# Kernel tuning notes

Hardware: AMD Instinct MI355X
Metric: run time of the kernel (lower is better)

## Reference

```python
import jax, jax.numpy as jnp
import numpy as np

B, S, I, R, O = 32, 4096, 64, 1024, 8
SPECTRAL_RADIUS = 0.95


def setup_inputs() -> dict:
    key = jax.random.key(0)
    k1, k2, k3, k4 = jax.random.split(key, 4)
    x = jax.random.normal(k1, (B, S, I), dtype=jnp.float32)
    W_in = jax.random.uniform(k2, (R, I), dtype=jnp.float32) - 0.5
    W_res = jax.random.uniform(k3, (R, R), dtype=jnp.float32) - 0.5
    # rescale W_res so its spectral radius equals SPECTRAL_RADIUS (as in __init__)
    radius = SPECTRAL_RADIUS / float(np.max(np.abs(np.linalg.eigvals(np.asarray(W_res)))))
    W_res = W_res * jnp.float32(radius)
    # original inits W_out to zeros; use small random values so output is non-trivial
    W_out = jax.random.normal(k4, (O, R + I), dtype=jnp.float32) * 0.02
    return {"x": x, "W_in": W_in, "W_res": W_res, "W_out": W_out}


def reference(x, W_in, W_res, W_out):
    # Precompute input drive for all timesteps: [B, S, R]
    pre = jnp.einsum('bsi,ri->bsr', x, W_in)

    def step(r, p_t):
        # r: [B, R], p_t: [B, R]
        r = jnp.tanh(p_t + r @ W_res.T)
        return r, r

    r0 = jnp.zeros((x.shape[0], W_res.shape[0]), dtype=x.dtype)
    _, rs = jax.lax.scan(step, r0, jnp.swapaxes(pre, 0, 1))  # rs: [S, B, R]
    rs = jnp.swapaxes(rs, 0, 1)                               # [B, S, R]
    feats = jnp.concatenate([x, rs], axis=-1)                 # [B, S, I+R]
    out = jnp.einsum('bsf,of->bso', feats, W_out)             # [B, S, O]
    return jnp.squeeze(out)
```

## Files before the change

### kernel.cpp

```cpp
#include <hip/hip_runtime.h>
#include <hip/hip_fp16.h>
#include <math.h>


#define NS 4096
#define NI 64
#define NR 1024
#define NO 8
#define NB 32
#define NGRP 8
#define GPP 32
#define CPG 4
#define WROWS 32
#define NT 512
#define XPAD 68

typedef __fp16 h2 __attribute__((ext_vector_type(2)));
union UH2 { unsigned u; h2 h; };

#define ATSU(p,v) __hip_atomic_store((p), (v), __ATOMIC_RELAXED, __HIP_MEMORY_SCOPE_AGENT)
#define ATLU(p)   __hip_atomic_load((p), __ATOMIC_RELAXED, __HIP_MEMORY_SCOPE_AGENT)
#define ATAU(p,v) __hip_atomic_fetch_add((p), (v), __ATOMIC_RELAXED, __HIP_MEMORY_SCOPE_AGENT)

static __device__ __forceinline__ h2 u2h(unsigned u) { UH2 t; t.u = u; return t.h; }

__global__ void init_cnt_kernel(unsigned int* cnt) {
  cnt[threadIdx.x] = 0u;
  cnt[threadIdx.x + 1024] = 0u;
}

__global__ __launch_bounds__(NT)
__attribute__((amdgpu_waves_per_eu(2, 2)))
void esn_scan(const float* __restrict__ x, const float* __restrict__ Win,
              const float* __restrict__ Wres, const float* __restrict__ Wout,
              float* __restrict__ out, unsigned int* __restrict__ cnt,
              unsigned int* __restrict__ rbuf_h)
{
  extern __shared__ float dynpad[];
  const int wg  = blockIdx.x;
  const int g   = wg & 7;
  const int m   = wg >> 3;
  const int tid = threadIdx.x;
  const int w   = tid >> 6;
  const int l   = tid & 63;

  __shared__ unsigned r_h[CPG][NR / 2];
  __shared__ float x_lds[3][CPG][XPAD];
  __shared__ float win_s[WROWS][XPAD];
  __shared__ unsigned woutr_h[NO][NR / 2];
  __shared__ float woutx_s[NO][NI];

  if (x[0] == 1234.5678f) { dynpad[tid] = 1.f; out[tid] = dynpad[tid ^ 1]; }

  h2 wh[32];
  {
    const int grow0 = 32 * m + 4 * w;
    #pragma unroll
    for (int r = 0; r < 4; ++r)
      #pragma unroll
      for (int s = 0; s < 4; ++s) {
        float4 t4 = *(const float4*)&Wres[(size_t)(grow0 + r) * NR + 4 * l + 256 * s];
        wh[(r * 4 + s) * 2 + 0] = __builtin_amdgcn_cvt_pkrtz(t4.x, t4.y);
        wh[(r * 4 + s) * 2 + 1] = __builtin_amdgcn_cvt_pkrtz(t4.z, t4.w);
      }
  }
  for (int idx = tid; idx < WROWS * NI; idx += NT) {
    int rr = idx >> 6, ii = idx & 63;
    win_s[rr][ii] = Win[(32 * m + rr) * NI + ii];
  }
  for (int idx = tid; idx < NO * (NR / 2); idx += NT) {
    int o = idx >> 9, p = idx & 511;
    UH2 t; t.h = __builtin_amdgcn_cvt_pkrtz(Wout[o * (NI + NR) + NI + 2 * p],
                                            Wout[o * (NI + NR) + NI + 2 * p + 1]);
    woutr_h[o][p] = t.u;
  }
  if (tid < NO * NI) {
    int o = tid >> 6, ii = tid & 63;
    woutx_s[o][ii] = Wout[o * (NI + NR) + ii];
  }
  if (tid < 256) {
    const int c = tid >> 6, ii = tid & 63;
    x_lds[0][c][ii] = x[(size_t)(4 * g + c) * NS * NI + ii];
  }
  __syncthreads();

  unsigned int* bcp = cnt + (g * 4 + (m & 3)) * 64;
  unsigned int* pol = cnt + g * 4 * 64;

  for (int t = 0; t < NS; ++t) {
    const int par = t & 1, pprev = par ^ 1;

    if (t > 0) {
      const unsigned* rq = rbuf_h + (size_t)pprev * NB * (NR / 2)
                                  + (size_t)(4 * g) * (NR / 2);
      unsigned uv[4];
      #pragma unroll
      for (int c = 0; c < 4; ++c) uv[c] = ATLU(rq + c * 512 + tid);
      #pragma unroll
      for (int c = 0; c < 4; ++c) r_h[c][tid] = uv[c];
    } else {
      #pragma unroll
      for (int c = 0; c < 4; ++c) r_h[c][tid] = 0u;
    }
    __syncthreads();

    float acc[4][4];
    #pragma unroll
    for (int r = 0; r < 4; ++r)
      #pragma unroll
      for (int c = 0; c < 4; ++c) acc[r][c] = 0.f;
    #pragma unroll
    for (int s = 0; s < 4; ++s) {
      uint2 q0 = *(const uint2*)&r_h[0][2 * l + 128 * s];
      uint2 q1 = *(const uint2*)&r_h[1][2 * l + 128 * s];
      uint2 q2 = *(const uint2*)&r_h[2][2 * l + 128 * s];
      uint2 q3 = *(const uint2*)&r_h[3][2 * l + 128 * s];
      #pragma unroll
      for (int r = 0; r < 4; ++r) {
        const h2 wa = wh[(r * 4 + s) * 2 + 0];
        const h2 wb = wh[(r * 4 + s) * 2 + 1];
        acc[r][0] = __builtin_amdgcn_fdot2(wa, u2h(q0.x), acc[r][0], false);
        acc[r][0] = __builtin_amdgcn_fdot2(wb, u2h(q0.y), acc[r][0], false);
        acc[r][1] = __builtin_amdgcn_fdot2(wa, u2h(q1.x), acc[r][1], false);
        acc[r][1] = __builtin_amdgcn_fdot2(wb, u2h(q1.y), acc[r][1], false);
        acc[r][2] = __builtin_amdgcn_fdot2(wa, u2h(q2.x), acc[r][2], false);
        acc[r][2] = __builtin_amdgcn_fdot2(wb, u2h(q2.y), acc[r][2], false);
        acc[r][3] = __builtin_amdgcn_fdot2(wa, u2h(q3.x), acc[r][3], false);
        acc[r][3] = __builtin_amdgcn_fdot2(wb, u2h(q3.y), acc[r][3], false);
      }
    }

    float v[16];
    #pragma unroll
    for (int k = 0; k < 16; ++k) v[k] = acc[k >> 2][k & 3];
    #pragma unroll
    for (int lev = 0; lev < 4; ++lev) {
      const int d = 1 << lev;
      const int n = 16 >> lev;
      #pragma unroll
      for (int i = 0; i < n / 2; ++i) {
        float a  = v[2 * i]     + __shfl_xor(v[2 * i],     d);
        float bb = v[2 * i + 1] + __shfl_xor(v[2 * i + 1], d);
        v[i] = (l & d) ? bb : a;
      }
    }
    float dsum = v[0];
    dsum += __shfl_xor(dsum, 16);
    dsum += __shfl_xor(dsum, 32);

    float pin;
    {
      const int p = l & 15;
      const int prow = 4 * w + (p >> 2);
      const int pc = p & 3;
      const int cb = (l >> 4) * 16;
      const float* wr = &win_s[prow][cb];
      const float* xr = &x_lds[t % 3][pc][cb];
      float4 a0 = *(const float4*)&wr[0];
      float4 a1 = *(const float4*)&wr[4];
      float4 a2 = *(const float4*)&wr[8];
      float4 a3 = *(const float4*)&wr[12];
      float4 b0 = *(const float4*)&xr[0];
      float4 b1 = *(const float4*)&xr[4];
      float4 b2 = *(const float4*)&xr[8];
      float4 b3 = *(const float4*)&xr[12];
      pin = a0.x * b0.x;
      pin = fmaf(a0.y, b0.y, pin); pin = fmaf(a0.z, b0.z, pin);
      pin = fmaf(a0.w, b0.w, pin);
      pin = fmaf(a1.x, b1.x, pin); pin = fmaf(a1.y, b1.y, pin);
      pin = fmaf(a1.z, b1.z, pin); pin = fmaf(a1.w, b1.w, pin);
      pin = fmaf(a2.x, b2.x, pin); pin = fmaf(a2.y, b2.y, pin);
      pin = fmaf(a2.z, b2.z, pin); pin = fmaf(a2.w, b2.w, pin);
      pin = fmaf(a3.x, b3.x, pin); pin = fmaf(a3.y, b3.y, pin);
      pin = fmaf(a3.z, b3.z, pin); pin = fmaf(a3.w, b3.w, pin);
      pin += __shfl_xor(pin, 16);
      pin += __shfl_xor(pin, 32);
    }

    {
      float rv = tanhf(dsum + pin);
      float rvo = __shfl_xor(rv, 4);
      if (l < 16 && ((l >> 2) & 1) == 0) {
        const int r = l >> 2, c = l & 3;
        UH2 hp; hp.h = __builtin_amdgcn_cvt_pkrtz(rv, rvo);
        const int pair = 16 * m + 2 * w + (r >> 1);
        ATSU(rbuf_h + (size_t)par * NB * (NR / 2)
                    + (size_t)(4 * g + c) * (NR / 2) + pair, hp.u);
      }
    }

    __syncthreads();
    if (tid == 0) ATAU(bcp, 1u);

    if (t + 1 < NS && tid < 256) {
      const int c = tid >> 6, ii = tid & 63;
      x_lds[(t + 1) % 3][c][ii] = x[((size_t)(4 * g + c) * NS + (t + 1)) * NI + ii];
    }
    if (t > 0 && m == ((t - 1) & 31)) {
      const int grp = tid >> 4;
      const int j   = tid & 15;
      const int c   = grp >> 3, o = grp & 7;
      float s = 0.f;
      #pragma unroll
      for (int k = 0; k < 16; ++k) {
        uint2 rr = *(const uint2*)&r_h[c][32 * k + 2 * j];
        uint2 ww = *(const uint2*)&woutr_h[o][32 * k + 2 * j];
        s = __builtin_amdgcn_fdot2(u2h(rr.x), u2h(ww.x), s, false);
        s = __builtin_amdgcn_fdot2(u2h(rr.y), u2h(ww.y), s, false);
      }
      #pragma unroll
      for (int e = 0; e < 4; ++e)
        s = fmaf(woutx_s[o][4 * j + e], x_lds[(t + 2) % 3][c][4 * j + e], s);
      s += __shfl_xor(s, 1); s += __shfl_xor(s, 2);
      s += __shfl_xor(s, 4); s += __shfl_xor(s, 8);
      if (j == 0) out[((size_t)(4 * g + c) * NS + (t - 1)) * NO + o] = s;
    }

    if (tid == 0) {
      const unsigned tg = 8u * (unsigned)(t + 1);
      for (;;) {
        unsigned u0 = ATLU(pol);
        unsigned u1 = ATLU(pol + 64);
        unsigned u2 = ATLU(pol + 128);
        unsigned u3 = ATLU(pol + 192);
        if (u0 >= tg && u1 >= tg && u2 >= tg && u3 >= tg) break;
      }
    }
    __syncthreads();
  }

  if (m == 31) {
    const int fpar = (NS - 1) & 1;
    const unsigned* rq = rbuf_h + (size_t)fpar * NB * (NR / 2)
                                + (size_t)(4 * g) * (NR / 2);
    unsigned uv[4];
    #pragma unroll
    for (int c = 0; c < 4; ++c) uv[c] = ATLU(rq + c * 512 + tid);
    #pragma unroll
    for (int c = 0; c < 4; ++c) r_h[c][tid] = uv[c];
    __syncthreads();
    const int grp = tid >> 4;
    const int j   = tid & 15;
    const int c   = grp >> 3, o = grp & 7;
    float s = 0.f;
    #pragma unroll
    for (int k = 0; k < 16; ++k) {
      uint2 rr = *(const uint2*)&r_h[c][32 * k + 2 * j];
      uint2 ww = *(const uint2*)&woutr_h[o][32 * k + 2 * j];
      s = __builtin_amdgcn_fdot2(u2h(rr.x), u2h(ww.x), s, false);
      s = __builtin_amdgcn_fdot2(u2h(rr.y), u2h(ww.y), s, false);
    }
    #pragma unroll
    for (int e = 0; e < 4; ++e)
      s = fmaf(woutx_s[o][4 * j + e], x_lds[(NS - 1) % 3][c][4 * j + e], s);
    s += __shfl_xor(s, 1); s += __shfl_xor(s, 2);
    s += __shfl_xor(s, 4); s += __shfl_xor(s, 8);
    if (j == 0) out[((size_t)(4 * g + c) * NS + (NS - 1)) * NO + o] = s;
  }
}

extern "C" void kernel_launch(void* const* d_in, const int* in_sizes, int n_in,
                              void* d_out, int out_size, void* d_ws, size_t ws_size,
                              hipStream_t stream) {
  const float* x    = (const float*)d_in[0];
  const float* Win  = (const float*)d_in[1];
  const float* Wres = (const float*)d_in[2];
  const float* Wout = (const float*)d_in[3];
  float* out = (float*)d_out;

  char* ws = (char*)d_ws;
  unsigned int* cnt = (unsigned int*)ws;
  unsigned int* rbuf_h = (unsigned int*)(ws + 8192);

  hipLaunchKernelGGL(init_cnt_kernel, dim3(1), dim3(1024), 0, stream, cnt);
  hipLaunchKernelGGL(esn_scan, dim3(256), dim3(NT), 64 * 1024, stream,
                     x, Win, Wres, Wout, out, cnt, rbuf_h);
}
```

Before: 10.12 ms.

## Interleave hidden-state buffer, widen barrier counters, overlap input GEMV, use fast tanh

The per-step hidden-state exchange buffer is interleaved across the 4 batch columns, so each thread reads 4 consecutive words instead of 4 strided ones. The inter-workgroup barrier goes from 4 counter slots per group to 8, each with fewer arrivals, and a whole wave polls them with a wave vote instead of one thread spinning. The x·W_in dot product is moved between the global load and the LDS store so it can hide the load latency. tanhf is replaced by an exp2/rcp approximation, which adds some rounding error.

```diff
diff --git a/kernel.cpp b/kernel.cpp
--- a/kernel.cpp
+++ b/kernel.cpp
@@ -14,6 +14,7 @@
 #define WROWS 32
 #define NT 512
 #define XPAD 68
+#define RPH (NB * NR / 2)
 
 typedef __fp16 h2 __attribute__((ext_vector_type(2)));
 union UH2 { unsigned u; h2 h; };
@@ -24,9 +25,15 @@
 
 static __device__ __forceinline__ h2 u2h(unsigned u) { UH2 t; t.u = u; return t.h; }
 
+static __device__ __forceinline__ float fast_tanh(float x) {
+  x = fminf(fmaxf(x, -20.f), 20.f);
+  float e = __builtin_amdgcn_exp2f(x * 2.8853900817779268f);
+  return (e - 1.0f) * __builtin_amdgcn_rcpf(e + 1.0f);
+}
+
 __global__ void init_cnt_kernel(unsigned int* cnt) {
-  cnt[threadIdx.x] = 0u;
-  cnt[threadIdx.x + 1024] = 0u;
+  const int t = threadIdx.x;
+  cnt[t] = 0u; cnt[t + 1024] = 0u; cnt[t + 2048] = 0u; cnt[t + 3072] = 0u;
 }
 
 __global__ __launch_bounds__(NT)
@@ -84,69 +91,19 @@
   }
   __syncthreads();
 
-  unsigned int* bcp = cnt + (g * 4 + (m & 3)) * 64;
-  unsigned int* pol = cnt + g * 4 * 64;
+  unsigned int* bcp = cnt + (g * 8 + (m & 7)) * 64;
 
   for (int t = 0; t < NS; ++t) {
     const int par = t & 1, pprev = par ^ 1;
 
+    unsigned uv0, uv1, uv2, uv3;
     if (t > 0) {
-      const unsigned* rq = rbuf_h + (size_t)pprev * NB * (NR / 2)
-                                  + (size_t)(4 * g) * (NR / 2);
-      unsigned uv[4];
-      #pragma unroll
-      for (int c = 0; c < 4; ++c) uv[c] = ATLU(rq + c * 512 + tid);
-      #pragma unroll
-      for (int c = 0; c < 4; ++c) r_h[c][tid] = uv[c];
+      const unsigned* rq = rbuf_h + (size_t)pprev * RPH + (size_t)g * 2048 + 4 * tid;
+      uv0 = ATLU(rq);     uv1 = ATLU(rq + 1);
+      uv2 = ATLU(rq + 2); uv3 = ATLU(rq + 3);
     } else {
-      #pragma unroll
-      for (int c = 0; c < 4; ++c) r_h[c][tid] = 0u;
-    }
-    __syncthreads();
-
-    float acc[4][4];
-    #pragma unroll
-    for (int r = 0; r < 4; ++r)
-      #pragma unroll
-      for (int c = 0; c < 4; ++c) acc[r][c] = 0.f;
-    #pragma unroll
-    for (int s = 0; s < 4; ++s) {
-      uint2 q0 = *(const uint2*)&r_h[0][2 * l + 128 * s];
-      uint2 q1 = *(const uint2*)&r_h[1][2 * l + 128 * s];
-      uint2 q2 = *(const uint2*)&r_h[2][2 * l + 128 * s];
-      uint2 q3 = *(const uint2*)&r_h[3][2 * l + 128 * s];
-      #pragma unroll
-      for (int r = 0; r < 4; ++r) {
-        const h2 wa = wh[(r * 4 + s) * 2 + 0];
-        const h2 wb = wh[(r * 4 + s) * 2 + 1];
-        acc[r][0] = __builtin_amdgcn_fdot2(wa, u2h(q0.x), acc[r][0], false);
-        acc[r][0] = __builtin_amdgcn_fdot2(wb, u2h(q0.y), acc[r][0], false);
-        acc[r][1] = __builtin_amdgcn_fdot2(wa, u2h(q1.x), acc[r][1], false);
-        acc[r][1] = __builtin_amdgcn_fdot2(wb, u2h(q1.y), acc[r][1], false);
-        acc[r][2] = __builtin_amdgcn_fdot2(wa, u2h(q2.x), acc[r][2], false);
-        acc[r][2] = __builtin_amdgcn_fdot2(wb, u2h(q2.y), acc[r][2], false);
-        acc[r][3] = __builtin_amdgcn_fdot2(wa, u2h(q3.x), acc[r][3], false);
-        acc[r][3] = __builtin_amdgcn_fdot2(wb, u2h(q3.y), acc[r][3], false);
-      }
-    }
-
-    float v[16];
-    #pragma unroll
-    for (int k = 0; k < 16; ++k) v[k] = acc[k >> 2][k & 3];
-    #pragma unroll
-    for (int lev = 0; lev < 4; ++lev) {
-      const int d = 1 << lev;
-      const int n = 16 >> lev;
-      #pragma unroll
-      for (int i = 0; i < n / 2; ++i) {
-        float a  = v[2 * i]     + __shfl_xor(v[2 * i],     d);
-        float bb = v[2 * i + 1] + __shfl_xor(v[2 * i + 1], d);
-        v[i] = (l & d) ? bb : a;
-      }
-    }
-    float dsum = v[0];
-    dsum += __shfl_xor(dsum, 16);
-    dsum += __shfl_xor(dsum, 32);
+      uv0 = uv1 = uv2 = uv3 = 0u;
+    }
 
     float pin;
     {
@@ -177,15 +134,62 @@
       pin += __shfl_xor(pin, 32);
     }
 
+    r_h[0][tid] = uv0; r_h[1][tid] = uv1;
+    r_h[2][tid] = uv2; r_h[3][tid] = uv3;
+    __syncthreads();
+
+    float acc[4][4];
+    #pragma unroll
+    for (int r = 0; r < 4; ++r)
+      #pragma unroll
+      for (int c = 0; c < 4; ++c) acc[r][c] = 0.f;
+    #pragma unroll
+    for (int s = 0; s < 4; ++s) {
+      uint2 q0 = *(const uint2*)&r_h[0][2 * l + 128 * s];
+      uint2 q1 = *(const uint2*)&r_h[1][2 * l + 128 * s];
+      uint2 q2 = *(const uint2*)&r_h[2][2 * l + 128 * s];
+      uint2 q3 = *(const uint2*)&r_h[3][2 * l + 128 * s];
+      #pragma unroll
+      for (int r = 0; r < 4; ++r) {
+        const h2 wa = wh[(r * 4 + s) * 2 + 0];
+        const h2 wb = wh[(r * 4 + s) * 2 + 1];
+        acc[r][0] = __builtin_amdgcn_fdot2(wa, u2h(q0.x), acc[r][0], false);
+        acc[r][0] = __builtin_amdgcn_fdot2(wb, u2h(q0.y), acc[r][0], false);
+        acc[r][1] = __builtin_amdgcn_fdot2(wa, u2h(q1.x), acc[r][1], false);
+        acc[r][1] = __builtin_amdgcn_fdot2(wb, u2h(q1.y), acc[r][1], false);
+        acc[r][2] = __builtin_amdgcn_fdot2(wa, u2h(q2.x), acc[r][2], false);
+        acc[r][2] = __builtin_amdgcn_fdot2(wb, u2h(q2.y), acc[r][2], false);
+        acc[r][3] = __builtin_amdgcn_fdot2(wa, u2h(q3.x), acc[r][3], false);
+        acc[r][3] = __builtin_amdgcn_fdot2(wb, u2h(q3.y), acc[r][3], false);
+      }
+    }
+
+    float v[16];
+    #pragma unroll
+    for (int k = 0; k < 16; ++k) v[k] = acc[k >> 2][k & 3];
+    #pragma unroll
+    for (int lev = 0; lev < 4; ++lev) {
+      const int d = 1 << lev;
+      const int n = 16 >> lev;
+      #pragma unroll
+      for (int i = 0; i < n / 2; ++i) {
+        float a  = v[2 * i]     + __shfl_xor(v[2 * i],     d);
+        float bb = v[2 * i + 1] + __shfl_xor(v[2 * i + 1], d);
+        v[i] = (l & d) ? bb : a;
+      }
+    }
+    float dsum = v[0];
+    dsum += __shfl_xor(dsum, 16);
+    dsum += __shfl_xor(dsum, 32);
+
     {
-      float rv = tanhf(dsum + pin);
+      float rv = fast_tanh(dsum + pin);
       float rvo = __shfl_xor(rv, 4);
       if (l < 16 && ((l >> 2) & 1) == 0) {
         const int r = l >> 2, c = l & 3;
         UH2 hp; hp.h = __builtin_amdgcn_cvt_pkrtz(rv, rvo);
         const int pair = 16 * m + 2 * w + (r >> 1);
-        ATSU(rbuf_h + (size_t)par * NB * (NR / 2)
-                    + (size_t)(4 * g + c) * (NR / 2) + pair, hp.u);
+        ATSU(rbuf_h + (size_t)par * RPH + (size_t)g * 2048 + 4 * pair + c, hp.u);
       }
     }
 
@@ -216,28 +220,21 @@
       if (j == 0) out[((size_t)(4 * g + c) * NS + (t - 1)) * NO + o] = s;
     }
 
-    if (tid == 0) {
-      const unsigned tg = 8u * (unsigned)(t + 1);
-      for (;;) {
-        unsigned u0 = ATLU(pol);
-        unsigned u1 = ATLU(pol + 64);
-        unsigned u2 = ATLU(pol + 128);
-        unsigned u3 = ATLU(pol + 192);
-        if (u0 >= tg && u1 >= tg && u2 >= tg && u3 >= tg) break;
-      }
+    if (w == 0) {
+      const unsigned tg = 4u * (unsigned)(t + 1);
+      const unsigned* pa = cnt + (g * 8 + (l & 7)) * 64;
+      while (!__all((int)(ATLU(pa) >= tg))) { }
     }
     __syncthreads();
   }
 
   if (m == 31) {
     const int fpar = (NS - 1) & 1;
-    const unsigned* rq = rbuf_h + (size_t)fpar * NB * (NR / 2)
-                                + (size_t)(4 * g) * (NR / 2);
-    unsigned uv[4];
-    #pragma unroll
-    for (int c = 0; c < 4; ++c) uv[c] = ATLU(rq + c * 512 + tid);
-    #pragma unroll
-    for (int c = 0; c < 4; ++c) r_h[c][tid] = uv[c];
+    const unsigned* rq = rbuf_h + (size_t)fpar * RPH + (size_t)g * 2048 + 4 * tid;
+    r_h[0][tid] = ATLU(rq);
+    r_h[1][tid] = ATLU(rq + 1);
+    r_h[2][tid] = ATLU(rq + 2);
+    r_h[3][tid] = ATLU(rq + 3);
     __syncthreads();
     const int grp = tid >> 4;
     const int j   = tid & 15;
@@ -270,7 +267,7 @@
 
   char* ws = (char*)d_ws;
   unsigned int* cnt = (unsigned int*)ws;
-  unsigned int* rbuf_h = (unsigned int*)(ws + 8192);
+  unsigned int* rbuf_h = (unsigned int*)(ws + 16384);
 
   hipLaunchKernelGGL(init_cnt_kernel, dim3(1), dim3(1024), 0, stream, cnt);
   hipLaunchKernelGGL(esn_scan, dim3(256), dim3(NT), 64 * 1024, stream,
```

Measured after the change: 11.16 ms. +10.3%, slower.
